# Kernel tuning notes

Measured on AMD Instinct MI355X. Metric: run time of the kernel, lower is better.

The kernel has to match this reference:

```python
import jax, jax.numpy as jnp
import numpy as np

N, E, FDIM, H = 50000, 1_600_000, 256, 128


def setup_inputs() -> dict:
    key = jax.random.key(0)
    ks = jax.random.split(key, 16)
    s = 0.05
    return {
        "node_features": jax.random.normal(ks[0], (N, FDIM), dtype=jnp.float32),
        "edge_index": jax.random.randint(ks[1], (2, E), 0, N, dtype=jnp.int64),
        # node encoder: Linear(F,H) -> ReLU -> Linear(H,H)
        "enc_w1": jax.random.normal(ks[2], (FDIM, H), dtype=jnp.float32) * s,
        "enc_b1": jnp.zeros((H,), dtype=jnp.float32),
        "enc_w2": jax.random.normal(ks[3], (H, H), dtype=jnp.float32) * s,
        "enc_b2": jnp.zeros((H,), dtype=jnp.float32),
        # three GCNConv layers (weight + bias each)
        "conv_w1": jax.random.normal(ks[4], (H, H), dtype=jnp.float32) * s,
        "conv_b1": jnp.zeros((H,), dtype=jnp.float32),
        "conv_w2": jax.random.normal(ks[5], (H, H), dtype=jnp.float32) * s,
        "conv_b2": jnp.zeros((H,), dtype=jnp.float32),
        "conv_w3": jax.random.normal(ks[6], (H, H), dtype=jnp.float32) * s,
        "conv_b3": jnp.zeros((H,), dtype=jnp.float32),
        # edge classifier: Linear(2H,H) -> ReLU -> Dropout(eval: identity) -> Linear(H,1) -> Sigmoid
        "cls_w1": jax.random.normal(ks[7], (2 * H, H), dtype=jnp.float32) * s,
        "cls_b1": jnp.zeros((H,), dtype=jnp.float32),
        "cls_w2": jax.random.normal(ks[8], (H, 1), dtype=jnp.float32) * s,
        "cls_b2": jnp.zeros((1,), dtype=jnp.float32),
    }


def _gcn_conv(x, w, b, src, dst, norm, n):
    # GCNConv: x' = scatter_add_dst(norm * (x W)[src]) + b  (self-loops already in src/dst/norm)
    xw = x @ w
    out = jax.ops.segment_sum(xw[src] * norm[:, None], dst, num_segments=n)
    return out + b


def reference(node_features, edge_index, enc_w1, enc_b1, enc_w2, enc_b2,
              conv_w1, conv_b1, conv_w2, conv_b2, conv_w3, conv_b3,
              cls_w1, cls_b1, cls_w2, cls_b2):
    n = node_features.shape[0]
    loops = jnp.arange(n, dtype=edge_index.dtype)
    src = jnp.concatenate([edge_index[0], loops])  # (E+N,)
    dst = jnp.concatenate([edge_index[1], loops])
    # symmetric normalization with self-loops (PyG gcn_norm defaults)
    deg = jax.ops.segment_sum(jnp.ones(src.shape, node_features.dtype), dst, num_segments=n)
    dis = jnp.where(deg > 0, jax.lax.rsqrt(jnp.maximum(deg, 1.0)), 0.0)
    norm = dis[src] * dis[dst]  # (E+N,)

    # node encoder
    x = jax.nn.relu(node_features @ enc_w1 + enc_b1) @ enc_w2 + enc_b2
    # stacked GCN layers
    x = jax.nn.relu(_gcn_conv(x, conv_w1, conv_b1, src, dst, norm, n))
    x = jax.nn.relu(_gcn_conv(x, conv_w2, conv_b2, src, dst, norm, n))
    x = _gcn_conv(x, conv_w3, conv_b3, src, dst, norm, n)

    # edge features: gather + concat  -> (E, 2H)
    ef = jnp.concatenate([x[edge_index[0]], x[edge_index[1]]], axis=1)
    h = jax.nn.relu(ef @ cls_w1 + cls_b1)  # Dropout is identity at eval
    scores = jax.nn.sigmoid(h @ cls_w2 + cls_b2)
    return scores.squeeze(-1)  # (E,)
```

## Files before the change

### kernel.cpp

```cpp
#include <hip/hip_runtime.h>
#include <math.h>

#define HDIM 128
#define BSH 7
#define MAXBUCK 512

typedef __attribute__((ext_vector_type(8))) short    bf16x8;
typedef __attribute__((ext_vector_type(4))) float    f32x4;
typedef __attribute__((ext_vector_type(2))) float    f32x2;
typedef __attribute__((ext_vector_type(8))) unsigned short u16x8;
typedef __attribute__((ext_vector_type(4))) unsigned short u16x4;

__device__ __forceinline__ float bf2f(unsigned short u) {
    union { unsigned int i; float f; } c; c.i = ((unsigned int)u) << 16; return c.f;
}
__device__ __forceinline__ unsigned short f2bf(float f) {
    union { float f; unsigned int i; } c; c.f = f;
    unsigned int r = (c.i + 0x7fffu + ((c.i >> 16) & 1u)) >> 16;
    return (unsigned short)r;
}
__device__ __forceinline__ void f8x8_dec(uint2 v, float* f) {
    f32x2 a = __builtin_amdgcn_cvt_pk_f32_fp8((int)v.x, false);
    f32x2 b = __builtin_amdgcn_cvt_pk_f32_fp8((int)v.x, true);
    f32x2 c = __builtin_amdgcn_cvt_pk_f32_fp8((int)v.y, false);
    f32x2 d = __builtin_amdgcn_cvt_pk_f32_fp8((int)v.y, true);
    f[0] = a.x; f[1] = a.y; f[2] = b.x; f[3] = b.y;
    f[4] = c.x; f[5] = c.y; f[6] = d.x; f[7] = d.y;
}

__global__ __launch_bounds__(256) void k_hist(
    const int* __restrict__ dst, int* __restrict__ tot,
    int* __restrict__ hist, int E, int chunk, int nbuck)
{
    __shared__ int h[MAXBUCK];
    for (int i = threadIdx.x; i < MAXBUCK; i += 256) h[i] = 0;
    __syncthreads();
    int beg = blockIdx.x * chunk;
    int fin = min(beg + chunk, E);
    for (int e = beg + threadIdx.x; e < fin; e += 256)
        atomicAdd(&h[dst[e] >> BSH], 1);
    __syncthreads();
    for (int k = threadIdx.x; k < nbuck; k += 256) {
        int v = h[k];
        hist[(size_t)blockIdx.x * nbuck + k] = v;
        if (v) atomicAdd(&tot[k], v);
    }
}

__global__ __launch_bounds__(256) void k_scan_buckets(
    const int* __restrict__ tot, int* __restrict__ gcur, int* __restrict__ base, int nbuck)
{
    __shared__ int a[MAXBUCK], b[MAXBUCK];
    int t = threadIdx.x;
    for (int i = t; i < MAXBUCK; i += 256) a[i] = (i < nbuck) ? tot[i] : 0;
    __syncthreads();
    int* s1 = a; int* s2 = b;
    for (int off = 1; off < MAXBUCK; off <<= 1) {
        for (int i = t; i < MAXBUCK; i += 256)
            s2[i] = s1[i] + ((i >= off) ? s1[i - off] : 0);
        __syncthreads();
        int* tmp = s1; s1 = s2; s2 = tmp;
    }
    for (int i = t; i < nbuck; i += 256) {
        int e = (i == 0) ? 0 : s1[i - 1];
        gcur[i] = e;
        base[i] = e;
    }
    if (t == 0) base[nbuck] = s1[nbuck - 1];
}

__global__ __launch_bounds__(256) void k_partition(
    const int* __restrict__ src, const int* __restrict__ dst,
    const int* __restrict__ hist, int* __restrict__ gcur,
    uint2* __restrict__ stag, int E, int chunk, int nbuck)
{
    __shared__ int h[MAXBUCK];
    int t = threadIdx.x;
    for (int k = t; k < nbuck; k += 256) {
        int v = hist[(size_t)blockIdx.x * nbuck + k];
        h[k] = v ? atomicAdd(&gcur[k], v) : 0;
    }
    __syncthreads();
    int beg = blockIdx.x * chunk;
    int fin = min(beg + chunk, E);
    for (int e = beg + t; e < fin; e += 256) {
        unsigned int d = (unsigned int)dst[e];
        unsigned int s = (unsigned int)src[e];
        int pos = atomicAdd(&h[d >> BSH], 1);
        stag[pos] = make_uint2(s | (d << 16), (unsigned int)e);
    }
}

__global__ __launch_bounds__(256) void k_bucket_csr(
    const int* __restrict__ base, const uint2* __restrict__ stag,
    int* __restrict__ row_ptr, int* __restrict__ col, float* __restrict__ dis, int n, int nbuck)
{
    __shared__ int cl[128], sa[128], sb[128], cur[128];
    int k = blockIdx.x;
    int n0 = k << BSH;
    int t = threadIdx.x;
    if (t < 128) cl[t] = 0;
    __syncthreads();
    int b0 = base[k];
    int m = base[k + 1] - b0;
    const uint2* seg = stag + b0;
    for (int i = t; i < m; i += 256) atomicAdd(&cl[(seg[i].x >> 16) & 127], 1);
    __syncthreads();
    int cv = 0;
    if (t < 128) { cv = cl[t]; sa[t] = cv; }
    __syncthreads();
    int* s1 = sa; int* s2 = sb;
    for (int off = 1; off < 128; off <<= 1) {
        if (t < 128) s2[t] = s1[t] + ((t >= off) ? s1[t - off] : 0);
        __syncthreads();
        int* tmp = s1; s1 = s2; s2 = tmp;
    }
    if (t < 128) {
        int node = n0 + t;
        if (node < n) {
            int rpv = b0 + s1[t] - cv;
            row_ptr[node] = rpv;
            cur[t] = rpv;
            dis[node] = rsqrtf(1.0f + (float)cv);
        }
    }
    if (k == 0 && t == 0) row_ptr[n] = base[nbuck];
    __syncthreads();
    for (int i = t; i < m; i += 256) {
        unsigned int e = seg[i].x;
        int pos = atomicAdd(&cur[(e >> 16) & 127], 1);
        col[pos] = (int)(e & 0xffffu);
    }
}

struct WEnt { const float* src; unsigned short* dst; int K; };
struct WAll { WEnt w[7]; };

__global__ __launch_bounds__(256) void k_prep_w(WAll all) {
    WEnt e = all.w[blockIdx.y];
    int i = blockIdx.x * 256 + threadIdx.x;
    if (i >= e.K * HDIM) return;
    int k = i >> 7, c = i & 127;
    e.dst[(size_t)c * e.K + k] = f2bf(e.src[i]);
}

__global__ __launch_bounds__(256) void k_gemm_b(
    const unsigned short* __restrict__ X, const unsigned short* __restrict__ Wt,
    const float* __restrict__ bias, const float* __restrict__ scale,
    void* __restrict__ C, int M, int relu_out, int out_fp8)
{
    const int K = 128;
    int wave = threadIdx.x >> 6, lane = threadIdx.x & 63;
    int quad = lane >> 4, r = lane & 15;
    int row0 = blockIdx.x * 64 + wave * 16;
    if (row0 >= M) return;
    const unsigned short* xp = X + (size_t)(row0 + r) * K + quad * 8;
    const unsigned short* wp = Wt + (size_t)r * K + quad * 8;
    f32x4 acc[8];
#pragma unroll
    for (int mt = 0; mt < 8; mt++) acc[mt] = (f32x4){0.f, 0.f, 0.f, 0.f};
#pragma unroll 2
    for (int k0 = 0; k0 < K; k0 += 32) {
        bf16x8 xf = *(const bf16x8*)(xp + k0);
#pragma unroll
        for (int mt = 0; mt < 8; mt++) {
            bf16x8 wf = *(const bf16x8*)(wp + (size_t)mt * 16 * K + k0);
            acc[mt] = __builtin_amdgcn_mfma_f32_16x16x32_bf16(wf, xf, acc[mt], 0, 0, 0);
        }
    }
    float sc = scale ? scale[row0 + r] : 1.f;
    if (out_fp8) {
        unsigned char* cp = (unsigned char*)C + (size_t)(row0 + r) * HDIM + quad * 4;
#pragma unroll
        for (int mt = 0; mt < 8; mt++) {
            float v[4];
#pragma unroll
            for (int j = 0; j < 4; j++) {
                float x = acc[mt][j];
                if (bias) x += bias[mt * 16 + quad * 4 + j];
                if (relu_out) x = fmaxf(x, 0.f);
                v[j] = x * sc;
            }
            int wd = 0;
            wd = __builtin_amdgcn_cvt_pk_fp8_f32(v[0], v[1], wd, false);
            wd = __builtin_amdgcn_cvt_pk_fp8_f32(v[2], v[3], wd, true);
            *(unsigned int*)(cp + mt * 16) = (unsigned int)wd;
        }
    } else {
        unsigned short* cp = (unsigned short*)C + (size_t)(row0 + r) * HDIM + quad * 4;
#pragma unroll
        for (int mt = 0; mt < 8; mt++) {
            u16x4 o;
#pragma unroll
            for (int j = 0; j < 4; j++) {
                float v = acc[mt][j];
                if (bias) v += bias[mt * 16 + quad * 4 + j];
                if (relu_out) v = fmaxf(v, 0.f);
                o[j] = f2bf(v * sc);
            }
            *(u16x4*)(cp + mt * 16) = o;
        }
    }
}

__global__ __launch_bounds__(256) void k_gemm_nf(
    const float* __restrict__ X, const unsigned short* __restrict__ Wt,
    const float* __restrict__ bias, unsigned short* __restrict__ C,
    int M, int relu_out)
{
    const int K = 256;
    int wave = threadIdx.x >> 6, lane = threadIdx.x & 63;
    int quad = lane >> 4, r = lane & 15;
    int row0 = blockIdx.x * 64 + wave * 16;
    if (row0 >= M) return;
    const float* xp = X + (size_t)(row0 + r) * K + quad * 8;
    const unsigned short* wp = Wt + (size_t)r * K + quad * 8;
    f32x4 acc[8];
#pragma unroll
    for (int mt = 0; mt < 8; mt++) acc[mt] = (f32x4){0.f, 0.f, 0.f, 0.f};
#pragma unroll 2
    for (int k0 = 0; k0 < K; k0 += 32) {
        float4 xa = *(const float4*)(xp + k0);
        float4 xb = *(const float4*)(xp + k0 + 4);
        bf16x8 xf;
        xf[0] = (short)f2bf(xa.x); xf[1] = (short)f2bf(xa.y);
        xf[2] = (short)f2bf(xa.z); xf[3] = (short)f2bf(xa.w);
        xf[4] = (short)f2bf(xb.x); xf[5] = (short)f2bf(xb.y);
        xf[6] = (short)f2bf(xb.z); xf[7] = (short)f2bf(xb.w);
#pragma unroll
        for (int mt = 0; mt < 8; mt++) {
            bf16x8 wf = *(const bf16x8*)(wp + (size_t)mt * 16 * K + k0);
            acc[mt] = __builtin_amdgcn_mfma_f32_16x16x32_bf16(wf, xf, acc[mt], 0, 0, 0);
        }
    }
    unsigned short* cp = C + (size_t)(row0 + r) * HDIM + quad * 4;
#pragma unroll
    for (int mt = 0; mt < 8; mt++) {
        u16x4 o;
#pragma unroll
        for (int j = 0; j < 4; j++) {
            float v = acc[mt][j];
            if (bias) v += bias[mt * 16 + quad * 4 + j];
            if (relu_out) v = fmaxf(v, 0.f);
            o[j] = f2bf(v);
        }
        *(u16x4*)(cp + mt * 16) = o;
    }
}

__global__ __launch_bounds__(256) void k_aggregate_f8(
    const int* __restrict__ row_ptr, const int* __restrict__ col,
    const float* __restrict__ dis, const uint2* __restrict__ y8,
    const float* __restrict__ bias, unsigned short* __restrict__ out, int n, int relu_out)
{
    int wid = (blockIdx.x * 256 + threadIdx.x) >> 6;
    if (wid >= n) return;
    int lane = threadIdx.x & 63;
    int q = lane >> 4, t = lane & 15;
    float acc[8];
    {
        uint2 sv = y8[(size_t)wid * 16 + t];
        float f[8]; f8x8_dec(sv, f);
#pragma unroll
        for (int i = 0; i < 8; i++) acc[i] = (q == 0) ? f[i] : 0.f;
    }
    int beg = row_ptr[wid], end = row_ptr[wid + 1];
    int j = beg + q;
    for (; j + 12 < end; j += 16) {
        int s0 = col[j], s1 = col[j + 4], s2 = col[j + 8], s3 = col[j + 12];
        uint2 v0 = y8[(size_t)s0 * 16 + t];
        uint2 v1 = y8[(size_t)s1 * 16 + t];
        uint2 v2 = y8[(size_t)s2 * 16 + t];
        uint2 v3 = y8[(size_t)s3 * 16 + t];
        float f0[8], f1[8], f2[8], f3[8];
        f8x8_dec(v0, f0); f8x8_dec(v1, f1); f8x8_dec(v2, f2); f8x8_dec(v3, f3);
#pragma unroll
        for (int i = 0; i < 8; i++) acc[i] += (f0[i] + f1[i]) + (f2[i] + f3[i]);
    }
    for (; j < end; j += 4) {
        int s = col[j];
        uint2 v = y8[(size_t)s * 16 + t];
        float f[8]; f8x8_dec(v, f);
#pragma unroll
        for (int i = 0; i < 8; i++) acc[i] += f[i];
    }
#pragma unroll
    for (int i = 0; i < 8; i++) {
        acc[i] += __shfl_xor(acc[i], 16, 64);
        acc[i] += __shfl_xor(acc[i], 32, 64);
    }
    if (q == 0) {
        float di = dis[wid];
        u16x8 o;
#pragma unroll
        for (int i = 0; i < 8; i++) {
            float v = di * acc[i] + bias[t * 8 + i];
            if (relu_out) v = fmaxf(v, 0.f);
            o[i] = f2bf(v);
        }
        *(u16x8*)(out + (size_t)wid * HDIM + t * 8) = o;
    }
}

__global__ __launch_bounds__(256) void k_edge_score_sorted(
    const uint2* __restrict__ stag, const uint2* __restrict__ P8,
    const uint2* __restrict__ Q8,
    const float* __restrict__ w2, const float* __restrict__ b2,
    float* __restrict__ out, int E, int chunk)
{
    int nblk = gridDim.x;
    int c = (int)((blockIdx.x & 7) * (nblk >> 3) + (blockIdx.x >> 3));
    int sub = threadIdx.x & 15;
    int grp = threadIdx.x >> 4;
    float w[8];
#pragma unroll
    for (int j = 0; j < 8; j++) w[j] = w2[sub * 8 + j];
    float bb = b2[0];
    int beg = c * chunk;
    int fin = min(beg + chunk, E);
    for (int i = beg + grp; i < fin; i += 16) {
        uint2 ent = stag[i];
        int s = (int)(ent.x & 0xffffu);
        int d = (int)(ent.x >> 16);
        uint2 pv = P8[(size_t)s * 16 + sub];
        uint2 qv = Q8[(size_t)d * 16 + sub];
        float pf[8], qf[8];
        f8x8_dec(pv, pf); f8x8_dec(qv, qf);
        float part = 0.f;
#pragma unroll
        for (int j = 0; j < 8; j++)
            part += fmaxf(pf[j] + qf[j], 0.f) * w[j];
        part += __shfl_xor(part, 8, 16);
        part += __shfl_xor(part, 4, 16);
        part += __shfl_xor(part, 2, 16);
        part += __shfl_xor(part, 1, 16);
        if (sub == 0) {
            float sc = 1.f / (1.f + expf(-(part + bb)));
            __builtin_nontemporal_store(sc, &out[ent.y]);
        }
    }
}

extern "C" void kernel_launch(void* const* d_in, const int* in_sizes, int n_in,
                              void* d_out, int out_size, void* d_ws, size_t ws_size,
                              hipStream_t stream) {
    const float* nf   = (const float*)d_in[0];
    const int*   ei   = (const int*)d_in[1];
    const float* ew1  = (const float*)d_in[2];
    const float* eb1  = (const float*)d_in[3];
    const float* ew2  = (const float*)d_in[4];
    const float* eb2  = (const float*)d_in[5];
    const float* cw1  = (const float*)d_in[6];
    const float* cb1  = (const float*)d_in[7];
    const float* cw2  = (const float*)d_in[8];
    const float* cb2  = (const float*)d_in[9];
    const float* cw3  = (const float*)d_in[10];
    const float* cb3  = (const float*)d_in[11];
    const float* clw1 = (const float*)d_in[12];
    const float* clb1 = (const float*)d_in[13];
    const float* clw2 = (const float*)d_in[14];
    const float* clb2 = (const float*)d_in[15];
    float* out = (float*)d_out;

    const int FD = 256;
    const int N = in_sizes[0] / FD;
    const int E = in_sizes[1] / 2;
    const int NBUCK = (N + 127) >> BSH;
    const int PBLK = 256;
    const int chunk = (E + PBLK - 1) / PBLK;

    size_t Np = ((size_t)N + 256) & ~(size_t)255;
    char* w = (char*)d_ws;
    float* dis     = (float*)w;            w += Np * 4;
    int*   tot     = (int*)w;              w += MAXBUCK * 4;
    int*   gcur    = (int*)w;              w += MAXBUCK * 4;
    int*   base    = (int*)w;              w += (MAXBUCK + 4) * 4;
    int*   hist    = (int*)w;              w += (size_t)PBLK * MAXBUCK * 4;
    int*   row_ptr = (int*)w;              w += Np * 4;
    uint2* stag    = (uint2*)w;            w += (size_t)E * 8;
    int*   col     = (int*)w;              w += (((size_t)E * 4) + 255) & ~(size_t)255;
    unsigned short* bufA = (unsigned short*)w;  w += (size_t)N * HDIM * 2;
    unsigned short* bufB = (unsigned short*)w;  w += (size_t)N * HDIM * 2;
    unsigned short* bufC = (unsigned short*)w;  w += (size_t)N * HDIM * 2;
    unsigned char*  f8X  = (unsigned char*)w;   w += ((size_t)N * HDIM + 255) & ~(size_t)255;
    unsigned char*  f8P  = (unsigned char*)w;   w += ((size_t)N * HDIM + 255) & ~(size_t)255;
    unsigned char*  f8Q  = (unsigned char*)w;   w += ((size_t)N * HDIM + 255) & ~(size_t)255;
    unsigned short* wtE1 = (unsigned short*)w;  w += 256 * HDIM * 2;
    unsigned short* wtE2 = (unsigned short*)w;  w += 128 * HDIM * 2;
    unsigned short* wtC1 = (unsigned short*)w;  w += 128 * HDIM * 2;
    unsigned short* wtC2 = (unsigned short*)w;  w += 128 * HDIM * 2;
    unsigned short* wtC3 = (unsigned short*)w;  w += 128 * HDIM * 2;
    unsigned short* wtT  = (unsigned short*)w;  w += 128 * HDIM * 2;
    unsigned short* wtB  = (unsigned short*)w;  w += 128 * HDIM * 2;

    int gemm_grid = (N + 63) / 64;
    int ag = (N + 3) / 4;

    WAll wa;
    wa.w[0] = { ew1,               wtE1, 256 };
    wa.w[1] = { ew2,               wtE2, 128 };
    wa.w[2] = { cw1,               wtC1, 128 };
    wa.w[3] = { cw2,               wtC2, 128 };
    wa.w[4] = { cw3,               wtC3, 128 };
    wa.w[5] = { clw1,              wtT,  128 };
    wa.w[6] = { clw1 + 128 * HDIM, wtB,  128 };
    k_prep_w<<<dim3(128, 7), 256, 0, stream>>>(wa);

    hipMemsetAsync(tot, 0, MAXBUCK * sizeof(int), stream);
    k_hist<<<PBLK, 256, 0, stream>>>(ei + E, tot, hist, E, chunk, NBUCK);
    k_scan_buckets<<<1, 256, 0, stream>>>(tot, gcur, base, NBUCK);
    k_partition<<<PBLK, 256, 0, stream>>>(ei, ei + E, hist, gcur, stag, E, chunk, NBUCK);
    k_bucket_csr<<<NBUCK, 256, 0, stream>>>(base, stag, row_ptr, col, dis, N, NBUCK);

    k_gemm_nf<<<gemm_grid, 256, 0, stream>>>(nf, wtE1, eb1, bufA, N, 1);
    k_gemm_b<<<gemm_grid, 256, 0, stream>>>(bufA, wtE2, eb2, nullptr, bufB, N, 0, 0);

    k_gemm_b<<<gemm_grid, 256, 0, stream>>>(bufB, wtC1, nullptr, dis, f8X, N, 0, 1);
    k_aggregate_f8<<<ag, 256, 0, stream>>>(row_ptr, col, dis, (const uint2*)f8X, cb1, bufC, N, 1);
    k_gemm_b<<<gemm_grid, 256, 0, stream>>>(bufC, wtC2, nullptr, dis, f8X, N, 0, 1);
    k_aggregate_f8<<<ag, 256, 0, stream>>>(row_ptr, col, dis, (const uint2*)f8X, cb2, bufA, N, 1);
    k_gemm_b<<<gemm_grid, 256, 0, stream>>>(bufA, wtC3, nullptr, dis, f8X, N, 0, 1);
    k_aggregate_f8<<<ag, 256, 0, stream>>>(row_ptr, col, dis, (const uint2*)f8X, cb3, bufB, N, 0);

    k_gemm_b<<<gemm_grid, 256, 0, stream>>>(bufB, wtT, clb1, nullptr, f8P, N, 0, 1);
    k_gemm_b<<<gemm_grid, 256, 0, stream>>>(bufB, wtB, nullptr, nullptr, f8Q, N, 0, 1);

    const int SBLK = 2048;
    int schunk = (E + SBLK - 1) / SBLK;
    k_edge_score_sorted<<<SBLK, 256, 0, stream>>>(stag, (const uint2*)f8P, (const uint2*)f8Q,
                                                  clw2, clb2, out, E, schunk);
}
```

Baseline: 542.2 us.

## Stage GEMM weights in LDS and unroll aggregation and edge-score loops deeper

```diff
diff --git a/kernel.cpp b/kernel.cpp
--- a/kernel.cpp
+++ b/kernel.cpp
@@ -149,22 +149,31 @@
     const float* __restrict__ bias, const float* __restrict__ scale,
     void* __restrict__ C, int M, int relu_out, int out_fp8)
 {
-    const int K = 128;
-    int wave = threadIdx.x >> 6, lane = threadIdx.x & 63;
+    __shared__ unsigned short sW[128 * 128];
+    const int t = threadIdx.x;
+#pragma unroll
+    for (int i = 0; i < 8; i++) {
+        int c = t + i * 256;
+        int row = c >> 4, o = c & 15;
+        int mt = row >> 4, r = row & 15, kc = o >> 2, q = o & 3;
+        int lidx = (mt * 4 + kc) * 64 + q * 16 + r;
+        *(uint4*)(sW + (size_t)lidx * 8) = *(const uint4*)(Wt + (size_t)c * 8);
+    }
+    __syncthreads();
+    int wave = t >> 6, lane = t & 63;
     int quad = lane >> 4, r = lane & 15;
     int row0 = blockIdx.x * 64 + wave * 16;
     if (row0 >= M) return;
-    const unsigned short* xp = X + (size_t)(row0 + r) * K + quad * 8;
-    const unsigned short* wp = Wt + (size_t)r * K + quad * 8;
+    const unsigned short* xp = X + (size_t)(row0 + r) * 128 + quad * 8;
     f32x4 acc[8];
 #pragma unroll
     for (int mt = 0; mt < 8; mt++) acc[mt] = (f32x4){0.f, 0.f, 0.f, 0.f};
-#pragma unroll 2
-    for (int k0 = 0; k0 < K; k0 += 32) {
-        bf16x8 xf = *(const bf16x8*)(xp + k0);
+#pragma unroll
+    for (int kc = 0; kc < 4; kc++) {
+        bf16x8 xf = *(const bf16x8*)(xp + kc * 32);
 #pragma unroll
         for (int mt = 0; mt < 8; mt++) {
-            bf16x8 wf = *(const bf16x8*)(wp + (size_t)mt * 16 * K + k0);
+            bf16x8 wf = *(const bf16x8*)(sW + ((size_t)((mt * 4 + kc) * 64 + lane)) * 8);
             acc[mt] = __builtin_amdgcn_mfma_f32_16x16x32_bf16(wf, xf, acc[mt], 0, 0, 0);
         }
     }
@@ -266,6 +275,20 @@
     }
     int beg = row_ptr[wid], end = row_ptr[wid + 1];
     int j = beg + q;
+    for (; j + 28 < end; j += 32) {
+        int s[8];
+        uint2 v[8];
+#pragma unroll
+        for (int u = 0; u < 8; u++) s[u] = col[j + u * 4];
+#pragma unroll
+        for (int u = 0; u < 8; u++) v[u] = y8[(size_t)s[u] * 16 + t];
+#pragma unroll
+        for (int u = 0; u < 8; u++) {
+            float f[8]; f8x8_dec(v[u], f);
+#pragma unroll
+            for (int i = 0; i < 8; i++) acc[i] += f[i];
+        }
+    }
     for (; j + 12 < end; j += 16) {
         int s0 = col[j], s1 = col[j + 4], s2 = col[j + 8], s3 = col[j + 12];
         uint2 v0 = y8[(size_t)s0 * 16 + t];
@@ -318,7 +341,36 @@
     float bb = b2[0];
     int beg = c * chunk;
     int fin = min(beg + chunk, E);
-    for (int i = beg + grp; i < fin; i += 16) {
+    int i = beg + grp;
+    for (; i + 16 < fin; i += 32) {
+        uint2 e0 = stag[i], e1 = stag[i + 16];
+        int s0 = (int)(e0.x & 0xffffu), d0 = (int)(e0.x >> 16);
+        int s1 = (int)(e1.x & 0xffffu), d1 = (int)(e1.x >> 16);
+        uint2 pv0 = P8[(size_t)s0 * 16 + sub];
+        uint2 qv0 = Q8[(size_t)d0 * 16 + sub];
+        uint2 pv1 = P8[(size_t)s1 * 16 + sub];
+        uint2 qv1 = Q8[(size_t)d1 * 16 + sub];
+        float pf0[8], qf0[8], pf1[8], qf1[8];
+        f8x8_dec(pv0, pf0); f8x8_dec(qv0, qf0);
+        f8x8_dec(pv1, pf1); f8x8_dec(qv1, qf1);
+        float p0 = 0.f, p1 = 0.f;
+#pragma unroll
+        for (int j = 0; j < 8; j++) {
+            p0 += fmaxf(pf0[j] + qf0[j], 0.f) * w[j];
+            p1 += fmaxf(pf1[j] + qf1[j], 0.f) * w[j];
+        }
+        p0 += __shfl_xor(p0, 8, 16); p1 += __shfl_xor(p1, 8, 16);
+        p0 += __shfl_xor(p0, 4, 16); p1 += __shfl_xor(p1, 4, 16);
+        p0 += __shfl_xor(p0, 2, 16); p1 += __shfl_xor(p1, 2, 16);
+        p0 += __shfl_xor(p0, 1, 16); p1 += __shfl_xor(p1, 1, 16);
+        if (sub == 0) {
+            float sc0 = 1.f / (1.f + expf(-(p0 + bb)));
+            float sc1 = 1.f / (1.f + expf(-(p1 + bb)));
+            __builtin_nontemporal_store(sc0, &out[e0.y]);
+            __builtin_nontemporal_store(sc1, &out[e1.y]);
+        }
+    }
+    if (i < fin) {
         uint2 ent = stag[i];
         int s = (int)(ent.x & 0xffffu);
         int d = (int)(ent.x >> 16);
```

Result: faster. 466.2 us (-14.0%).
